# Kernel optimization log

Measured on AMD Instinct MI355X. Metric: run time of the kernel, lower is better.

## Reference

```python
import jax, jax.numpy as jnp
import numpy as np

N_NODES = 100_000
N_EDGES = 1_600_000
IN_C, OUT_C = 128, 64


def setup_inputs() -> dict:
    key = jax.random.key(0)
    k1, k2, k3, k4 = jax.random.split(key, 4)
    x = jax.random.normal(k1, (N_NODES, IN_C), dtype=jnp.float32)
    # xavier_uniform with relu gain sqrt(2)
    gain = float(np.sqrt(2.0))
    bound = gain * float(np.sqrt(6.0 / (IN_C + OUT_C)))
    weight = jax.random.uniform(k2, (IN_C, OUT_C), minval=-bound, maxval=bound, dtype=jnp.float32)
    bias = jnp.zeros((OUT_C,), dtype=jnp.float32)
    src = jax.random.randint(k3, (N_EDGES,), 0, N_NODES, dtype=jnp.int32)
    dst = jax.random.randint(k4, (N_EDGES,), 0, N_NODES, dtype=jnp.int32)
    return {"x": x, "weight": weight, "bias": bias, "src": src, "dst": dst}


def reference(x, weight, bias, src, dst):
    # DGL GraphConv, norm='both'.
    n = x.shape[0]
    ones = jnp.ones(src.shape, dtype=x.dtype)
    deg_out = jax.ops.segment_sum(ones, src, num_segments=n)  # source out-degree
    deg_in = jax.ops.segment_sum(ones, dst, num_segments=n)   # destination in-degree
    norm_src = jnp.maximum(deg_out, 1.0) ** -0.5
    norm_dst = jnp.maximum(deg_in, 1.0) ** -0.5
    h = x * norm_src[:, None]          # [N, IN]
    # in_channels > out_channels: apply weight before aggregation (DGL fast path)
    h = h @ weight                      # [N, OUT]
    msg = h[src]                        # [E, OUT] gather
    agg = jax.ops.segment_sum(msg, dst, num_segments=n)  # [N, OUT] scatter-add
    return agg * norm_dst[:, None] + bias
```

## Files before the change

kernel.cpp:

```cpp
#include <hip/hip_runtime.h>
#include <hip/hip_bf16.h>

#define N_NODES 100000
#define N_EDGES 1600000
#define IN_C    128
#define OUT_C   64

#define SLOT_W 48
#define CAP    47

typedef __bf16 bf16x8 __attribute__((ext_vector_type(8)));
typedef float  f32x4  __attribute__((ext_vector_type(4)));

#define DEGS_OFF  0
#define CNT_OFF   400000
#define SLOT_OFF  800000
#define H_OFF     20000000

__global__ __launch_bounds__(256) void fill_kernel(
    const int* __restrict__ src, const int* __restrict__ dst,
    int* __restrict__ degs, int* __restrict__ cnt, int* __restrict__ slots) {
  const int i = blockIdx.x * 256 + threadIdx.x;
  if (i * 2 >= N_EDGES) return;
  const int2 s2 = *(const int2*)(src + i * 2);
  const int2 d2 = *(const int2*)(dst + i * 2);
  atomicAdd(&degs[s2.x], 1);
  atomicAdd(&degs[s2.y], 1);
  const int p0 = atomicAdd(&cnt[d2.x], 1);
  if (p0 < CAP) slots[d2.x * SLOT_W + p0] = s2.x;
  const int p1 = atomicAdd(&cnt[d2.y], 1);
  if (p1 < CAP) slots[d2.y * SLOT_W + p1] = s2.y;
}

__global__ __launch_bounds__(256) void gemm_kernel(
    const float* __restrict__ x, const float* __restrict__ w,
    const int* __restrict__ degs, __bf16* __restrict__ h) {
  const int lane = threadIdx.x & 63;
  const int l15 = lane & 15;
  const int q = lane >> 4;
  const int g = blockIdx.x * 4 + (threadIdx.x >> 6);
  if (g >= N_NODES / 16) return;

  bf16x8 bfrag[4][4];
#pragma unroll
  for (int kc = 0; kc < 4; ++kc) {
#pragma unroll
    for (int t = 0; t < 4; ++t) {
      bf16x8 tmp;
#pragma unroll
      for (int j = 0; j < 8; ++j)
        tmp[j] = (__bf16)w[(kc * 32 + q * 8 + j) * OUT_C + t * 16 + l15];
      bfrag[kc][t] = tmp;
    }
  }

  const int n0 = g * 16;
  const float* xp = x + (long)(n0 + l15) * IN_C + q * 8;

  f32x4 acc[4];
#pragma unroll
  for (int t = 0; t < 4; ++t) {
    f32x4 z = {0.f, 0.f, 0.f, 0.f};
    acc[t] = z;
  }

#pragma unroll
  for (int kc = 0; kc < 4; ++kc) {
    f32x4 u = *(const f32x4*)(xp + kc * 32);
    f32x4 v = *(const f32x4*)(xp + kc * 32 + 4);
    bf16x8 a;
#pragma unroll
    for (int j = 0; j < 4; ++j) {
      a[j] = (__bf16)u[j];
      a[4 + j] = (__bf16)v[j];
    }
#pragma unroll
    for (int t = 0; t < 4; ++t)
      acc[t] = __builtin_amdgcn_mfma_f32_16x16x32_bf16(a, bfrag[kc][t], acc[t], 0, 0, 0);
  }

#pragma unroll
  for (int r = 0; r < 4; ++r) {
    const int row = n0 + q * 4 + r;
    const int d = degs[row];
    const float s = rsqrtf((float)(d < 1 ? 1 : d));
#pragma unroll
    for (int t = 0; t < 4; ++t)
      h[(long)row * OUT_C + t * 16 + l15] = (__bf16)(acc[t][r] * s);
  }
}

__global__ __launch_bounds__(256) void aggregate_kernel(
    const __bf16* __restrict__ h, const int* __restrict__ cnt,
    const int* __restrict__ slots, const float* __restrict__ bias,
    float* __restrict__ out) {
  const int node = blockIdx.x * 4 + (threadIdx.x >> 6);
  if (node >= N_NODES) return;
  const int lane = threadIdx.x & 63;
  const int eg = lane >> 3;
  const int c8 = (lane & 7) * 8;

  const int c = cnt[node];
  const float ndv = rsqrtf((float)(c < 1 ? 1 : c));
  const int end = c < CAP ? c : CAP;
  const int* sl = slots + (long)node * SLOT_W;

  float acc[8];
#pragma unroll
  for (int k = 0; k < 8; ++k) acc[k] = 0.f;

  for (int j = 0; j < end; j += 8) {
    const int e = j + eg;
    if (e < end) {
      const int s = sl[e];
      bf16x8 v = *(const bf16x8*)(h + (long)s * OUT_C + c8);
#pragma unroll
      for (int k = 0; k < 8; ++k) acc[k] += (float)v[k];
    }
  }

#pragma unroll
  for (int mask = 8; mask <= 32; mask <<= 1) {
#pragma unroll
    for (int k = 0; k < 8; ++k)
      acc[k] += __shfl_xor(acc[k], mask, 64);
  }

  if (lane < 8) {
    f32x4 r0, r1;
#pragma unroll
    for (int k = 0; k < 4; ++k) {
      r0[k] = acc[k] * ndv + bias[c8 + k];
      r1[k] = acc[4 + k] * ndv + bias[c8 + 4 + k];
    }
    float* op = out + (long)node * OUT_C + c8;
    *(f32x4*)op = r0;
    *(f32x4*)(op + 4) = r1;
  }
}

extern "C" void kernel_launch(void* const* d_in, const int* in_sizes, int n_in,
                              void* d_out, int out_size, void* d_ws, size_t ws_size,
                              hipStream_t stream) {
  const float* x    = (const float*)d_in[0];
  const float* w    = (const float*)d_in[1];
  const float* bias = (const float*)d_in[2];
  const int*   src  = (const int*)d_in[3];
  const int*   dst  = (const int*)d_in[4];
  float* out = (float*)d_out;

  char* ws = (char*)d_ws;
  int*    degs  = (int*)(ws + DEGS_OFF);
  int*    cnt   = (int*)(ws + CNT_OFF);
  int*    slots = (int*)(ws + SLOT_OFF);
  __bf16* h     = (__bf16*)(ws + H_OFF);

  hipMemsetAsync(ws, 0, 2 * N_NODES * sizeof(int), stream);

  fill_kernel<<<(N_EDGES / 2 + 255) / 256, 256, 0, stream>>>(
      src, dst, degs, cnt, slots);

  gemm_kernel<<<(N_NODES / 16 + 3) / 4, 256, 0, stream>>>(x, w, degs, h);

  aggregate_kernel<<<(N_NODES + 3) / 4, 256, 0, stream>>>(
      h, cnt, slots, bias, out);
}
```

Baseline: 314.4 us.

## Compute source degrees via LDS privatized histogram instead of global atomics

```diff
diff --git a/kernel.cpp b/kernel.cpp
--- a/kernel.cpp
+++ b/kernel.cpp
@@ -9,6 +9,11 @@
 #define SLOT_W 48
 #define CAP    47
 
+#define HIST_BINS 16384
+#define HIST_R    7
+#define HIST_C    24
+#define HIST_CH   66672
+
 typedef __bf16 bf16x8 __attribute__((ext_vector_type(8)));
 typedef float  f32x4  __attribute__((ext_vector_type(4)));
 
@@ -17,19 +22,65 @@
 #define SLOT_OFF  800000
 #define H_OFF     20000000
 
+__global__ __launch_bounds__(256) void hist_kernel(
+    const int* __restrict__ src, int* __restrict__ partial) {
+  __shared__ int hist[HIST_BINS];
+  const int r = blockIdx.x / HIST_C;
+  const int c = blockIdx.x % HIST_C;
+  const int base = r * HIST_BINS;
+  for (int i = threadIdx.x; i < HIST_BINS; i += 256) hist[i] = 0;
+  __syncthreads();
+
+  const int lo = c * HIST_CH;
+  const int hi = (lo + HIST_CH < N_EDGES) ? lo + HIST_CH : N_EDGES;
+  for (int i = lo + threadIdx.x * 16; i < hi; i += 256 * 16) {
+    if (i + 16 <= hi) {
+      int4 a = *(const int4*)(src + i);
+      int4 b = *(const int4*)(src + i + 4);
+      int4 d = *(const int4*)(src + i + 8);
+      int4 e = *(const int4*)(src + i + 12);
+      int v[16] = {a.x, a.y, a.z, a.w, b.x, b.y, b.z, b.w,
+                   d.x, d.y, d.z, d.w, e.x, e.y, e.z, e.w};
+#pragma unroll
+      for (int k = 0; k < 16; ++k) {
+        int u = v[k] - base;
+        if ((unsigned)u < HIST_BINS) atomicAdd(&hist[u], 1);
+      }
+    } else {
+      for (int j = i; j < hi; ++j) {
+        int u = src[j] - base;
+        if ((unsigned)u < HIST_BINS) atomicAdd(&hist[u], 1);
+      }
+    }
+  }
+  __syncthreads();
+  int* out = partial + (long)blockIdx.x * HIST_BINS;
+  for (int i = threadIdx.x; i < HIST_BINS; i += 256) out[i] = hist[i];
+}
+
+__global__ __launch_bounds__(256) void hist_reduce_kernel(
+    const int* __restrict__ partial, int* __restrict__ degs) {
+  const int i = blockIdx.x * 256 + threadIdx.x;
+  if (i >= N_NODES) return;
+  const int r = i >> 14;
+  const int u = i & (HIST_BINS - 1);
+  const int* p = partial + (long)r * HIST_C * HIST_BINS + u;
+  int s = 0;
+#pragma unroll
+  for (int c = 0; c < HIST_C; ++c) s += p[(long)c * HIST_BINS];
+  degs[i] = s;
+}
+
 __global__ __launch_bounds__(256) void fill_kernel(
     const int* __restrict__ src, const int* __restrict__ dst,
-    int* __restrict__ degs, int* __restrict__ cnt, int* __restrict__ slots) {
+    int* __restrict__ cnt, int* __restrict__ slots) {
   const int i = blockIdx.x * 256 + threadIdx.x;
-  if (i * 2 >= N_EDGES) return;
-  const int2 s2 = *(const int2*)(src + i * 2);
-  const int2 d2 = *(const int2*)(dst + i * 2);
-  atomicAdd(&degs[s2.x], 1);
-  atomicAdd(&degs[s2.y], 1);
-  const int p0 = atomicAdd(&cnt[d2.x], 1);
-  if (p0 < CAP) slots[d2.x * SLOT_W + p0] = s2.x;
-  const int p1 = atomicAdd(&cnt[d2.y], 1);
-  if (p1 < CAP) slots[d2.y * SLOT_W + p1] = s2.y;
+  if (i < N_EDGES) {
+    const int s = src[i];
+    const int d = dst[i];
+    const int pos = atomicAdd(&cnt[d], 1);
+    if (pos < CAP) slots[d * SLOT_W + pos] = s;
+  }
 }
 
 __global__ __launch_bounds__(256) void gemm_kernel(
@@ -150,17 +201,20 @@
   float* out = (float*)d_out;
 
   char* ws = (char*)d_ws;
-  int*    degs  = (int*)(ws + DEGS_OFF);
-  int*    cnt   = (int*)(ws + CNT_OFF);
-  int*    slots = (int*)(ws + SLOT_OFF);
-  __bf16* h     = (__bf16*)(ws + H_OFF);
-
-  hipMemsetAsync(ws, 0, 2 * N_NODES * sizeof(int), stream);
-
-  fill_kernel<<<(N_EDGES / 2 + 255) / 256, 256, 0, stream>>>(
-      src, dst, degs, cnt, slots);
+  int*    degs    = (int*)(ws + DEGS_OFF);
+  int*    cnt     = (int*)(ws + CNT_OFF);
+  int*    slots   = (int*)(ws + SLOT_OFF);
+  __bf16* h       = (__bf16*)(ws + H_OFF);
+  int*    partial = (int*)(ws + H_OFF);
+
+  hipMemsetAsync(ws + CNT_OFF, 0, N_NODES * sizeof(int), stream);
+
+  hist_kernel<<<HIST_R * HIST_C, 256, 0, stream>>>(src, partial);
+  hist_reduce_kernel<<<(N_NODES + 255) / 256, 256, 0, stream>>>(partial, degs);
 
   gemm_kernel<<<(N_NODES / 16 + 3) / 4, 256, 0, stream>>>(x, w, degs, h);
+
+  fill_kernel<<<(N_EDGES + 255) / 256, 256, 0, stream>>>(src, dst, cnt, slots);
 
   aggregate_kernel<<<(N_NODES + 3) / 4, 256, 0, stream>>>(
       h, cnt, slots, bias, out);
```

After: 306.1 us. 1.03x faster.
